# Performance work log

Hardware: AMD Instinct MI355X
Metric: run time of the kernel (lower is better)

Reference implementation:

```python
import jax, jax.numpy as jnp
import numpy as np

N, X_DIM, Y_DIM, HID = 1024, 256, 256, 256  # HID = hidden_size // 2


def setup_inputs() -> dict:
    key = jax.random.key(0)
    ks = jax.random.split(key, 11)
    s_in = 1.0 / np.sqrt(X_DIM)
    s_h = 1.0 / np.sqrt(HID)
    return {
        "x_samples": jax.random.normal(ks[0], (N, X_DIM), jnp.float32),
        "y_samples": jax.random.normal(ks[1], (N, Y_DIM), jnp.float32),
        "z_samples": jax.random.normal(ks[2], (N, Y_DIM), jnp.float32),
        "w1_mu": jax.random.uniform(ks[3], (HID, X_DIM), jnp.float32, -s_in, s_in),
        "b1_mu": jax.random.uniform(ks[4], (HID,), jnp.float32, -s_in, s_in),
        "w2_mu": jax.random.uniform(ks[5], (Y_DIM, HID), jnp.float32, -s_h, s_h),
        "b2_mu": jax.random.uniform(ks[6], (Y_DIM,), jnp.float32, -s_h, s_h),
        "w1_lv": jax.random.uniform(ks[7], (HID, X_DIM), jnp.float32, -s_in, s_in),
        "b1_lv": jax.random.uniform(ks[8], (HID,), jnp.float32, -s_in, s_in),
        "w2_lv": jax.random.uniform(ks[9], (Y_DIM, HID), jnp.float32, -s_h, s_h),
        "b2_lv": jax.random.uniform(ks[10], (Y_DIM,), jnp.float32, -s_h, s_h),
    }


def reference(x_samples, y_samples, z_samples,
              w1_mu, b1_mu, w2_mu, b2_mu,
              w1_lv, b1_lv, w2_lv, b2_lv):
    # MLP heads (torch Linear: x @ W.T + b)
    h_mu = jax.nn.relu(x_samples @ w1_mu.T + b1_mu)
    mu = h_mu @ w2_mu.T + b2_mu                       # [N, D]
    h_lv = jax.nn.relu(x_samples @ w1_lv.T + b1_lv)
    logvar = jnp.tanh(h_lv @ w2_lv.T + b2_lv)          # [N, D]

    inv2var = 1.0 / (2.0 * jnp.exp(logvar))           # [N, D]

    # positive: per-sample conditional log-density term
    positive = -((mu - y_samples) ** 2 + (mu - z_samples) ** 2) * inv2var  # [N, D]

    # negative: mean over all pairings (i: prediction, j: sample)
    # pairwise squared diffs materialize [N, N, D] like the original broadcast
    pred = mu[:, None, :]                              # [N, 1, D]
    sq = (y_samples[None, :, :] - pred) ** 2 + (z_samples[None, :, :] - pred) ** 2
    negative = -sq.mean(axis=1) * inv2var              # [N, D]

    return jax.nn.relu(positive.sum(axis=-1) - negative.sum(axis=-1)).mean()
```

## Files before the change

kernel.cpp:

```cpp
#include <hip/hip_runtime.h>
#include <math.h>

constexpr int BT = 64;
constexpr int KT = 64;
constexpr int LS = 68;

template <bool SUMRELU_A>
__device__ __forceinline__ void gemm_tile_sk(const float* __restrict__ A0,
                                             const float* __restrict__ A1,
                                             const float* __restrict__ B,
                                             const float* __restrict__ bias,
                                             float* __restrict__ C,
                                             int rowBase, int colBase, int k0) {
    const int t = threadIdx.x;
    const int tx = t & 15;
    const int ty = t >> 4;

    __shared__ float As[KT][LS];
    __shared__ float Bs[KT][LS];

    float acc[4][4] = {};

    for (int kt = k0; kt < k0 + 128; kt += KT) {
#pragma unroll
        for (int p = 0; p < 4; p++) {
            int idx = p * 256 + t;
            int r = idx >> 4;
            int k4 = idx & 15;
            int off = (rowBase + r) * 256 + kt + k4 * 4;
            float4 av = *(const float4*)&A0[off];
            if (SUMRELU_A) {
                float4 a1 = *(const float4*)&A1[off];
                av.x = fmaxf(av.x + a1.x, 0.f);
                av.y = fmaxf(av.y + a1.y, 0.f);
                av.z = fmaxf(av.z + a1.z, 0.f);
                av.w = fmaxf(av.w + a1.w, 0.f);
            }
            float4 bv = *(const float4*)&B[(colBase + r) * 256 + kt + k4 * 4];
            As[k4 * 4 + 0][r] = av.x; As[k4 * 4 + 1][r] = av.y;
            As[k4 * 4 + 2][r] = av.z; As[k4 * 4 + 3][r] = av.w;
            Bs[k4 * 4 + 0][r] = bv.x; Bs[k4 * 4 + 1][r] = bv.y;
            Bs[k4 * 4 + 2][r] = bv.z; Bs[k4 * 4 + 3][r] = bv.w;
        }
        __syncthreads();

#pragma unroll 16
        for (int k = 0; k < KT; k++) {
            float4 a4 = *(const float4*)&As[k][ty * 4];
            float4 b4 = *(const float4*)&Bs[k][tx * 4];
            float av[4] = {a4.x, a4.y, a4.z, a4.w};
            float bv[4] = {b4.x, b4.y, b4.z, b4.w};
#pragma unroll
            for (int i = 0; i < 4; i++)
#pragma unroll
                for (int j = 0; j < 4; j++)
                    acc[i][j] = fmaf(av[i], bv[j], acc[i][j]);
        }
        __syncthreads();
    }

    float bb[4] = {0.f, 0.f, 0.f, 0.f};
    if (bias) {
        float4 bq = *(const float4*)&bias[colBase + tx * 4];
        bb[0] = bq.x; bb[1] = bq.y; bb[2] = bq.z; bb[3] = bq.w;
    }
#pragma unroll
    for (int i = 0; i < 4; i++) {
        int row = rowBase + ty * 4 + i;
        float4 o;
        o.x = acc[i][0] + bb[0];
        o.y = acc[i][1] + bb[1];
        o.z = acc[i][2] + bb[2];
        o.w = acc[i][3] + bb[3];
        *(float4*)&C[row * 256 + colBase + tx * 4] = o;
    }
}

#define DECODE_GEMM(bid, chunk, head, rowBase, colBase, k0) \
    int chunk = (bid) & 1;                                  \
    int head  = ((bid) >> 1) & 1;                           \
    int colBase = (((bid) >> 2) & 3) * BT;                  \
    int rowBase = ((bid) >> 4) * BT;                        \
    int k0 = chunk * 128;

__global__ __launch_bounds__(256)
void k1_layer1_moments(const float* __restrict__ x,
                       const float* __restrict__ w1m, const float* __restrict__ w1l,
                       const float* __restrict__ b1m, const float* __restrict__ b1l,
                       float* __restrict__ hm0, float* __restrict__ hm1,
                       float* __restrict__ hl0, float* __restrict__ hl1,
                       const float* __restrict__ y, const float* __restrict__ z,
                       float* __restrict__ pA, float* __restrict__ pB,
                       float* __restrict__ out) {
    int bid = blockIdx.x;
    if (bid < 256) {
        DECODE_GEMM(bid, chunk, head, rowBase, colBase, k0)
        const float* B = head ? w1l : w1m;
        const float* bias = chunk ? nullptr : (head ? b1l : b1m);
        float* C = head ? (chunk ? hl1 : hl0) : (chunk ? hm1 : hm0);
        gemm_tile_sk<false>(x, nullptr, B, bias, C, rowBase, colBase, k0);
    } else {
        int m = bid - 256;
        int t = threadIdx.x;
        float sA = 0.f, sB = 0.f;
        int base = m * 64 * 256 + t;
#pragma unroll 8
        for (int j = 0; j < 64; j++) {
            float yv = y[base + j * 256];
            float zv = z[base + j * 256];
            sA += yv * yv + zv * zv;
            sB += yv + zv;
        }
        pA[m * 256 + t] = sA;
        pB[m * 256 + t] = sB;
        if (m == 0 && t == 0) out[0] = 0.f;
    }
}

__global__ __launch_bounds__(256)
void k2_layer2(const float* __restrict__ hm0, const float* __restrict__ hm1,
               const float* __restrict__ hl0, const float* __restrict__ hl1,
               const float* __restrict__ w2m, const float* __restrict__ w2l,
               const float* __restrict__ b2m, const float* __restrict__ b2l,
               float* __restrict__ mu0, float* __restrict__ mu1,
               float* __restrict__ lv0, float* __restrict__ lv1) {
    int bid = blockIdx.x;
    DECODE_GEMM(bid, chunk, head, rowBase, colBase, k0)
    const float* A0 = head ? hl0 : hm0;
    const float* A1 = head ? hl1 : hm1;
    const float* B = head ? w2l : w2m;
    const float* bias = chunk ? nullptr : (head ? b2l : b2m);
    float* C = head ? (chunk ? lv1 : lv0) : (chunk ? mu1 : mu0);
    gemm_tile_sk<true>(A0, A1, B, bias, C, rowBase, colBase, k0);
}

__global__ __launch_bounds__(256)
void k3_epilogue(const float* __restrict__ mu0, const float* __restrict__ mu1,
                 const float* __restrict__ lv0, const float* __restrict__ lv1,
                 const float* __restrict__ y, const float* __restrict__ z,
                 const float* __restrict__ pA, const float* __restrict__ pB,
                 float* __restrict__ out) {
    __shared__ float red[4];
    int t = threadIdx.x;
    int lane = t & 63, wave = t >> 6;
    int row0 = blockIdx.x * 4;

    float mA = 0.f, mB = 0.f;
#pragma unroll
    for (int m = 0; m < 16; m++) {
        mA += pA[m * 256 + t];
        mB += pB[m * 256 + t];
    }
    mA *= (1.f / 1024.f);
    mB *= (1.f / 1024.f);

    float blockSum = 0.f;
    for (int r = 0; r < 4; r++) {
        int i = row0 + r;
        int o = i * 256 + t;
        float m  = mu0[o] + mu1[o];
        float lv = tanhf(lv0[o] + lv1[o]);
        float iv = 0.5f * expf(-lv);
        float yv = y[o];
        float zv = z[o];
        float Mt = mA - 2.f * m * mB + 2.f * m * m;
        float dy = m - yv, dz = m - zv;
        float term = iv * (Mt - dy * dy - dz * dz);
#pragma unroll
        for (int mask = 32; mask; mask >>= 1)
            term += __shfl_xor(term, mask, 64);
        if (lane == 0) red[wave] = term;
        __syncthreads();
        if (t == 0) {
            float rs = red[0] + red[1] + red[2] + red[3];
            blockSum += fmaxf(rs, 0.f);
        }
        __syncthreads();
    }
    if (t == 0) atomicAdd(out, blockSum * (1.f / 1024.f));
}

extern "C" void kernel_launch(void* const* d_in, const int* in_sizes, int n_in,
                              void* d_out, int out_size, void* d_ws, size_t ws_size,
                              hipStream_t stream) {
    const float* x   = (const float*)d_in[0];
    const float* y   = (const float*)d_in[1];
    const float* zs  = (const float*)d_in[2];
    const float* w1m = (const float*)d_in[3];
    const float* b1m = (const float*)d_in[4];
    const float* w2m = (const float*)d_in[5];
    const float* b2m = (const float*)d_in[6];
    const float* w1l = (const float*)d_in[7];
    const float* b1l = (const float*)d_in[8];
    const float* w2l = (const float*)d_in[9];
    const float* b2l = (const float*)d_in[10];
    float* out = (float*)d_out;

    char* ws = (char*)d_ws;
    float* pA  = (float*)(ws);
    float* pB  = (float*)(ws + (16u << 10));
    float* buf = (float*)(ws + (64u << 10));
    const unsigned MB = (1u << 20) / 4;
    float* hm0 = buf + 0 * MB;
    float* hm1 = buf + 1 * MB;
    float* hl0 = buf + 2 * MB;
    float* hl1 = buf + 3 * MB;
    float* mu0 = buf + 4 * MB;
    float* mu1 = buf + 5 * MB;
    float* lv0 = buf + 6 * MB;
    float* lv1 = buf + 7 * MB;

    k1_layer1_moments<<<272, 256, 0, stream>>>(x, w1m, w1l, b1m, b1l,
                                               hm0, hm1, hl0, hl1,
                                               y, zs, pA, pB, out);
    k2_layer2<<<256, 256, 0, stream>>>(hm0, hm1, hl0, hl1,
                                       w2m, w2l, b2m, b2l,
                                       mu0, mu1, lv0, lv1);
    k3_epilogue<<<256, 256, 0, stream>>>(mu0, mu1, lv0, lv1,
                                         y, zs, pA, pB, out);
}
```

Measured before the change: 105.7 us.

## Swizzle LDS tiles and distribute y/z moment reduction across GEMM blocks

Applies an XOR-free rotational swizzle to the shared-memory A/B tiles so the transposed stores and float4 reads hit different banks. Removes the 16 extra moment-reduction blocks from the first kernel and instead has each GEMM block reduce four rows of y/z, with a second partial reduction folded into the layer-2 kernel. This aims to cut LDS bank conflicts and the tail from long serial reduction blocks, at the cost of extra workspace and a two-stage reduction.

```diff
diff --git a/kernel.cpp b/kernel.cpp
--- a/kernel.cpp
+++ b/kernel.cpp
@@ -37,17 +37,20 @@
                 av.w = fmaxf(av.w + a1.w, 0.f);
             }
             float4 bv = *(const float4*)&B[(colBase + r) * 256 + kt + k4 * 4];
-            As[k4 * 4 + 0][r] = av.x; As[k4 * 4 + 1][r] = av.y;
-            As[k4 * 4 + 2][r] = av.z; As[k4 * 4 + 3][r] = av.w;
-            Bs[k4 * 4 + 0][r] = bv.x; Bs[k4 * 4 + 1][r] = bv.y;
-            Bs[k4 * 4 + 2][r] = bv.z; Bs[k4 * 4 + 3][r] = bv.w;
+            int rs = (r + 4 * k4) & 63;
+            As[k4 * 4 + 0][rs] = av.x; As[k4 * 4 + 1][rs] = av.y;
+            As[k4 * 4 + 2][rs] = av.z; As[k4 * 4 + 3][rs] = av.w;
+            Bs[k4 * 4 + 0][rs] = bv.x; Bs[k4 * 4 + 1][rs] = bv.y;
+            Bs[k4 * 4 + 2][rs] = bv.z; Bs[k4 * 4 + 3][rs] = bv.w;
         }
         __syncthreads();
 
 #pragma unroll 16
         for (int k = 0; k < KT; k++) {
-            float4 a4 = *(const float4*)&As[k][ty * 4];
-            float4 b4 = *(const float4*)&Bs[k][tx * 4];
+            int sa = (ty * 4 + (k & ~3)) & 63;
+            int sb = (tx * 4 + (k & ~3)) & 63;
+            float4 a4 = *(const float4*)&As[k][sa];
+            float4 b4 = *(const float4*)&Bs[k][sb];
             float av[4] = {a4.x, a4.y, a4.z, a4.w};
             float bv[4] = {b4.x, b4.y, b4.z, b4.w};
 #pragma unroll
@@ -84,37 +87,34 @@
     int k0 = chunk * 128;
 
 __global__ __launch_bounds__(256)
-void k1_layer1_moments(const float* __restrict__ x,
-                       const float* __restrict__ w1m, const float* __restrict__ w1l,
-                       const float* __restrict__ b1m, const float* __restrict__ b1l,
-                       float* __restrict__ hm0, float* __restrict__ hm1,
-                       float* __restrict__ hl0, float* __restrict__ hl1,
-                       const float* __restrict__ y, const float* __restrict__ z,
-                       float* __restrict__ pA, float* __restrict__ pB,
-                       float* __restrict__ out) {
+void k1_layer1(const float* __restrict__ x,
+               const float* __restrict__ w1m, const float* __restrict__ w1l,
+               const float* __restrict__ b1m, const float* __restrict__ b1l,
+               float* __restrict__ hm0, float* __restrict__ hm1,
+               float* __restrict__ hl0, float* __restrict__ hl1,
+               const float* __restrict__ y, const float* __restrict__ z,
+               float* __restrict__ pA1, float* __restrict__ pB1,
+               float* __restrict__ out) {
     int bid = blockIdx.x;
-    if (bid < 256) {
-        DECODE_GEMM(bid, chunk, head, rowBase, colBase, k0)
-        const float* B = head ? w1l : w1m;
-        const float* bias = chunk ? nullptr : (head ? b1l : b1m);
-        float* C = head ? (chunk ? hl1 : hl0) : (chunk ? hm1 : hm0);
-        gemm_tile_sk<false>(x, nullptr, B, bias, C, rowBase, colBase, k0);
-    } else {
-        int m = bid - 256;
-        int t = threadIdx.x;
-        float sA = 0.f, sB = 0.f;
-        int base = m * 64 * 256 + t;
-#pragma unroll 8
-        for (int j = 0; j < 64; j++) {
-            float yv = y[base + j * 256];
-            float zv = z[base + j * 256];
-            sA += yv * yv + zv * zv;
-            sB += yv + zv;
-        }
-        pA[m * 256 + t] = sA;
-        pB[m * 256 + t] = sB;
-        if (m == 0 && t == 0) out[0] = 0.f;
-    }
+    int t = threadIdx.x;
+    DECODE_GEMM(bid, chunk, head, rowBase, colBase, k0)
+    const float* Bw = head ? w1l : w1m;
+    const float* bias = chunk ? nullptr : (head ? b1l : b1m);
+    float* C = head ? (chunk ? hl1 : hl0) : (chunk ? hm1 : hm0);
+    gemm_tile_sk<false>(x, nullptr, Bw, bias, C, rowBase, colBase, k0);
+
+    float sA = 0.f, sB = 0.f;
+    int base = bid * 4 * 256 + t;
+#pragma unroll
+    for (int j = 0; j < 4; j++) {
+        float yv = y[base + j * 256];
+        float zv = z[base + j * 256];
+        sA += yv * yv + zv * zv;
+        sB += yv + zv;
+    }
+    pA1[bid * 256 + t] = sA;
+    pB1[bid * 256 + t] = sB;
+    if (bid == 0 && t == 0) out[0] = 0.f;
 }
 
 __global__ __launch_bounds__(256)
@@ -123,41 +123,54 @@
                const float* __restrict__ w2m, const float* __restrict__ w2l,
                const float* __restrict__ b2m, const float* __restrict__ b2l,
                float* __restrict__ mu0, float* __restrict__ mu1,
-               float* __restrict__ lv0, float* __restrict__ lv1) {
+               float* __restrict__ lv0, float* __restrict__ lv1,
+               const float* __restrict__ pA1, const float* __restrict__ pB1,
+               float* __restrict__ pA2, float* __restrict__ pB2) {
     int bid = blockIdx.x;
+    int t = threadIdx.x;
     DECODE_GEMM(bid, chunk, head, rowBase, colBase, k0)
     const float* A0 = head ? hl0 : hm0;
     const float* A1 = head ? hl1 : hm1;
-    const float* B = head ? w2l : w2m;
+    const float* Bw = head ? w2l : w2m;
     const float* bias = chunk ? nullptr : (head ? b2l : b2m);
     float* C = head ? (chunk ? lv1 : lv0) : (chunk ? mu1 : mu0);
-    gemm_tile_sk<true>(A0, A1, B, bias, C, rowBase, colBase, k0);
+    gemm_tile_sk<true>(A0, A1, Bw, bias, C, rowBase, colBase, k0);
+
+    if (bid < 16) {
+        float sA = 0.f, sB = 0.f;
+#pragma unroll
+        for (int s = 0; s < 16; s++) {
+            int o = (bid * 16 + s) * 256 + t;
+            sA += pA1[o];
+            sB += pB1[o];
+        }
+        pA2[bid * 256 + t] = sA;
+        pB2[bid * 256 + t] = sB;
+    }
 }
 
 __global__ __launch_bounds__(256)
 void k3_epilogue(const float* __restrict__ mu0, const float* __restrict__ mu1,
                  const float* __restrict__ lv0, const float* __restrict__ lv1,
                  const float* __restrict__ y, const float* __restrict__ z,
-                 const float* __restrict__ pA, const float* __restrict__ pB,
+                 const float* __restrict__ pA2, const float* __restrict__ pB2,
                  float* __restrict__ out) {
     __shared__ float red[4];
     int t = threadIdx.x;
     int lane = t & 63, wave = t >> 6;
-    int row0 = blockIdx.x * 4;
 
     float mA = 0.f, mB = 0.f;
 #pragma unroll
-    for (int m = 0; m < 16; m++) {
-        mA += pA[m * 256 + t];
-        mB += pB[m * 256 + t];
+    for (int g = 0; g < 16; g++) {
+        mA += pA2[g * 256 + t];
+        mB += pB2[g * 256 + t];
     }
     mA *= (1.f / 1024.f);
     mB *= (1.f / 1024.f);
 
     float blockSum = 0.f;
     for (int r = 0; r < 4; r++) {
-        int i = row0 + r;
-        int o = i * 256 + t;
+        int o = (blockIdx.x * 4 + r) * 256 + t;
         float m  = mu0[o] + mu1[o];
         float lv = tanhf(lv0[o] + lv1[o]);
         float iv = 0.5f * expf(-lv);
@@ -197,9 +210,11 @@
     float* out = (float*)d_out;
 
     char* ws = (char*)d_ws;
-    float* pA  = (float*)(ws);
-    float* pB  = (float*)(ws + (16u << 10));
-    float* buf = (float*)(ws + (64u << 10));
+    float* pA2 = (float*)(ws);
+    float* pB2 = (float*)(ws + (16u << 10));
+    float* pA1 = (float*)(ws + (256u << 10));
+    float* pB1 = (float*)(ws + (512u << 10));
+    float* buf = (float*)(ws + (1u << 20));
     const unsigned MB = (1u << 20) / 4;
     float* hm0 = buf + 0 * MB;
     float* hm1 = buf + 1 * MB;
@@ -210,12 +225,13 @@
     float* lv0 = buf + 6 * MB;
     float* lv1 = buf + 7 * MB;
 
-    k1_layer1_moments<<<272, 256, 0, stream>>>(x, w1m, w1l, b1m, b1l,
-                                               hm0, hm1, hl0, hl1,
-                                               y, zs, pA, pB, out);
+    k1_layer1<<<256, 256, 0, stream>>>(x, w1m, w1l, b1m, b1l,
+                                       hm0, hm1, hl0, hl1,
+                                       y, zs, pA1, pB1, out);
     k2_layer2<<<256, 256, 0, stream>>>(hm0, hm1, hl0, hl1,
                                        w2m, w2l, b2m, b2l,
-                                       mu0, mu1, lv0, lv1);
+                                       mu0, mu1, lv0, lv1,
+                                       pA1, pB1, pA2, pB2);
     k3_epilogue<<<256, 256, 0, stream>>>(mu0, mu1, lv0, lv1,
-                                         y, zs, pA, pB, out);
-}
+                                         y, zs, pA2, pB2, out);
+}
```

Result: no change. 104.8 us (-0.9%).
